# Optimization experiments

Hardware: AMD Instinct MI355X
Metric: run time of the kernel (lower is better)

## Reference

```python
import jax, jax.numpy as jnp
import numpy as np

HEAD = 8
C = 32  # dhead
SCALE = 0.17677669529663687  # 1/sqrt(32)


def setup_inputs() -> dict:
    key = jax.random.key(0)
    k1, k2, k3, k4 = jax.random.split(key, 4)
    N, S, R, M = 1, 256, 384, 256
    msa_repr = jax.random.normal(k1, (N, S, R, M), dtype=jnp.float32)
    # 0.02 init scale keeps softmax logits / sigmoid pre-activations in a sane range
    gate_proj = jax.random.normal(k2, (M, M), dtype=jnp.float32) * 0.02
    qkv_proj = jax.random.normal(k3, (M, 3 * M), dtype=jnp.float32) * 0.02
    out_proj = jax.random.normal(k4, (M, M), dtype=jnp.float32) * 0.02
    return {"msa_repr": msa_repr, "gate_proj": gate_proj, "qkv_proj": qkv_proj, "out_proj": out_proj}


def reference(msa_repr, gate_proj, qkv_proj, out_proj):
    # col_attn: permute [N,S,R,M] -> [N,R,S,M]; attention runs over the residue axis S
    x = jnp.transpose(msa_repr, (0, 2, 1, 3))  # [N,R,S,M]
    N, R, S, M = x.shape
    gate = jax.nn.sigmoid(x @ gate_proj).reshape(N, R, S, HEAD, C)
    q, k, v = jnp.split(x @ qkv_proj, 3, axis=-1)  # each [N,R,S,M]
    q = q.reshape(N, R, S, HEAD, C)
    k = k.reshape(N, R, S, HEAD, C)
    v = v.reshape(N, R, S, HEAD, C)
    sim = jnp.einsum('nrihc,nrjhc->nrhij', q, k) * jnp.float32(SCALE)  # [N,R,H,S,S]
    attn = jax.nn.softmax(sim, axis=-1)
    out = jnp.einsum('nrhij,nrjhc->nrihc', attn, v) * gate  # [N,R,S,H,C]
    out = out.reshape(N, R, S, HEAD * C) @ out_proj  # [N,R,S,M]
    return jnp.transpose(out, (0, 2, 1, 3))  # back to [N,S,R,M]
```

## Files before the change

### kernel.cpp

```cpp
#include <hip/hip_runtime.h>
#include <hip/hip_bf16.h>

#define R_DIM 384
#define S_DIM 256
#define M_DIM 256

typedef __attribute__((ext_vector_type(4))) float  f32x4;
typedef __attribute__((ext_vector_type(4))) float  fvec4;
typedef __attribute__((ext_vector_type(8))) short  short8;
typedef __attribute__((ext_vector_type(4))) short  short4v;

__device__ __forceinline__ short f2bf(float f) {
    __hip_bfloat16 h = __float2bfloat16(f);
    return __builtin_bit_cast(short, h);
}
__device__ __forceinline__ float bf2f(short s) {
    return __bfloat162float(__builtin_bit_cast(__hip_bfloat16, s));
}

#define QSCALE (0.17677669529663687f * 1.4426950408889634f)

__global__ __launch_bounds__(256) void k_prep(
    const float* __restrict__ gp, const float* __restrict__ qkvp,
    const float* __restrict__ op, short* __restrict__ Wt1,
    short* __restrict__ Wot)
{
    __shared__ float tile[64][65];
    const int tx = threadIdx.x & 63, ty = threadIdx.x >> 6;
    const int k0 = blockIdx.x * 64;
    const int j0 = blockIdx.y * 64;
    const float* src; int ld, cb;
    if (j0 < 256)       { src = gp;   ld = 256; cb = j0; }
    else if (j0 < 1024) { src = qkvp; ld = 768; cb = j0 - 256; }
    else                { src = op;   ld = 256; cb = j0 - 1024; }
    for (int q = 0; q < 16; ++q) {
        const int kk = q * 4 + ty;
        tile[kk][tx] = src[(k0 + kk) * ld + cb + tx];
    }
    __syncthreads();
    for (int q = 0; q < 16; ++q) {
        const int jj = q * 4 + ty;
        const int jglob = j0 + jj;
        const float scl = (jglob >= 256 && jglob < 512) ? QSCALE : 1.0f;
        const float val = tile[tx][jj] * scl;
        if (jglob < 1024) Wt1[jglob * 256 + k0 + tx] = f2bf(val);
        else              Wot[(jglob - 1024) * 256 + k0 + tx] = f2bf(val);
    }
}

__global__ __launch_bounds__(256) void k_qkvgate(
    const float* __restrict__ msa, const short* __restrict__ Wt1,
    short* __restrict__ gate, short* __restrict__ qb,
    short* __restrict__ kb, short* __restrict__ vb)
{
    __shared__ __align__(16) char Al[128 * 512];
    __shared__ __align__(16) char Bl[128 * 128];
    const int tid = threadIdx.x;
    const int l = tid & 63, w = tid >> 6;
    const int wr = w >> 1, wc = w & 1;
    const int rowBase = blockIdx.x * 128;

    {
        const int arow0 = tid >> 6;
        const int col4  = (tid & 63) * 4;
        const int slot  = (tid & 63) >> 1;
        const int sub   = (tid & 63) & 1;
        for (int ii = 0; ii < 32; ++ii) {
            const int a_r = ii * 4 + arow0;
            const int i = rowBase + a_r;
            const int rr = i >> 8, ss = i & 255;
            fvec4 vv = *(const fvec4*)(msa + ((ss * R_DIM + rr) << 8) + col4);
            short4v b4;
            b4.x = f2bf(vv.x); b4.y = f2bf(vv.y);
            b4.z = f2bf(vv.z); b4.w = f2bf(vv.w);
            *(short4v*)(Al + a_r * 512 + ((slot ^ (a_r & 7)) << 4) + sub * 8) = b4;
        }
    }
    __syncthreads();

    for (int ct = 0; ct < 8; ++ct) {
        const int colBase = ct * 128;
        f32x4 acc[4][4] = {};
        for (int kidx = 0; kidx < 4; ++kidx) {
            const int k0 = kidx * 64;
            {
                const int slotB = tid & 7;
                const int jb = tid >> 3;
                #pragma unroll
                for (int jj = 0; jj < 4; ++jj) {
                    const int j_r = jj * 32 + jb;
                    short8 wv = *(const short8*)(Wt1 + (colBase + j_r) * 256 + k0 + slotB * 8);
                    *(short8*)(Bl + j_r * 128 + ((slotB ^ (j_r & 7)) << 4)) = wv;
                }
            }
            __syncthreads();
            #pragma unroll
            for (int kh = 0; kh < 2; ++kh) {
                short8 af[4], bfr[4];
                const int aslot = kidx * 8 + kh * 4 + (l >> 4);
                const int bslot = kh * 4 + (l >> 4);
                #pragma unroll
                for (int it = 0; it < 4; ++it) {
                    const int row = wr * 64 + it * 16 + (l & 15);
                    af[it] = *(const short8*)(Al + row * 512 + ((aslot ^ (row & 7)) << 4));
                }
                #pragma unroll
                for (int jt = 0; jt < 4; ++jt) {
                    const int row = wc * 64 + jt * 16 + (l & 15);
                    bfr[jt] = *(const short8*)(Bl + row * 128 + ((bslot ^ (row & 7)) << 4));
                }
                #pragma unroll
                for (int it = 0; it < 4; ++it)
                    #pragma unroll
                    for (int jt = 0; jt < 4; ++jt)
                        acc[it][jt] = __builtin_amdgcn_mfma_f32_16x16x32_bf16(
                            af[it], bfr[jt], acc[it][jt], 0, 0, 0);
            }
            __syncthreads();
        }
        const int sel = ct >> 1;
        short* dst = (sel == 0) ? gate : (sel == 1) ? qb : (sel == 2) ? kb : vb;
        #pragma unroll
        for (int it = 0; it < 4; ++it) {
            const int base_i = rowBase + wr * 64 + it * 16 + ((l >> 4) << 2);
            #pragma unroll
            for (int reg = 0; reg < 4; ++reg) {
                const int i = base_i + reg;
                const int rr = i >> 8, ss = i & 255;
                #pragma unroll
                for (int jt = 0; jt < 4; ++jt) {
                    const int jg = colBase + wc * 64 + jt * 16 + (l & 15);
                    const int jj = jg & 255;
                    const int h = jj >> 5, c = jj & 31;
                    float vv = acc[it][jt][reg];
                    if (sel == 0) vv = 1.0f / (1.0f + __builtin_amdgcn_exp2f(-vv * 1.4426950408889634f));
                    dst[(((rr << 3) + h) * 256 + ss) * 32 + c] = f2bf(vv);
                }
            }
        }
    }
}

__global__ __launch_bounds__(256) void k_attn(
    short* qo, const short* __restrict__ kb, const short* __restrict__ vb,
    const short* __restrict__ gate)
{
    __shared__ __align__(16) short Kl[256 * 36];
    __shared__ __align__(16) short Vt[32 * 264];
    __shared__ __align__(16) short Pl[4 * 32 * 68];
    const int tid = threadIdx.x;
    const int l = tid & 63, w = tid >> 6;
    const int p = blockIdx.x;
    short* qg = qo + p * 8192;
    const short* kg = kb + p * 8192;
    const short* vg = vb + p * 8192;
    const short* gg = gate + p * 8192;

    short8 qf[4];
    {
        const int c0 = (l >> 4) * 8;
        #pragma unroll
        for (int it = 0; it < 4; ++it) {
            const int s = w * 64 + it * 16 + (l & 15);
            qf[it] = *(const short8*)(qg + s * 32 + c0);
        }
    }
    for (int itr = 0; itr < 4; ++itr) {
        const int idx = itr * 256 + tid;
        const int s = idx >> 2, slot = idx & 3;
        short8 kv = *(const short8*)(kg + s * 32 + slot * 8);
        *(short8*)(&Kl[s * 36 + slot * 8]) = kv;
    }
    for (int itr = 0; itr < 4; ++itr) {
        const int idx = itr * 256 + tid;
        const int s = idx >> 2, c0 = (idx & 3) * 8;
        short8 vv = *(const short8*)(vg + s * 32 + c0);
        #pragma unroll
        for (int e = 0; e < 8; ++e) Vt[(c0 + e) * 264 + s] = vv[e];
    }
    __syncthreads();

    f32x4 oacc[4][2] = {};
    f32x4 ssum[4] = {};
    short8 bones;
    #pragma unroll
    for (int e = 0; e < 8; ++e) bones[e] = (short)0x3F80;
    short* Pw = &Pl[w * (32 * 68)];

    for (int ch = 0; ch < 4; ++ch) {
        const int j0 = ch * 64;
        f32x4 sacc[4][4] = {};
        short8 kf[4];
        #pragma unroll
        for (int jt = 0; jt < 4; ++jt) {
            const int row = j0 + jt * 16 + (l & 15);
            kf[jt] = *(const short8*)(&Kl[row * 36 + (l >> 4) * 8]);
        }
        #pragma unroll
        for (int it = 0; it < 4; ++it)
            #pragma unroll
            for (int jt = 0; jt < 4; ++jt)
                sacc[it][jt] = __builtin_amdgcn_mfma_f32_16x16x32_bf16(
                    qf[it], kf[jt], sacc[it][jt], 0, 0, 0);

        short8 vfa[2][2];
        #pragma unroll
        for (int kk = 0; kk < 2; ++kk)
            #pragma unroll
            for (int cti = 0; cti < 2; ++cti)
                vfa[kk][cti] = *(const short8*)(
                    &Vt[(cti * 16 + (l & 15)) * 264 + j0 + kk * 32 + (l >> 4) * 8]);

        #pragma unroll
        for (int ih = 0; ih < 2; ++ih) {
            #pragma unroll
            for (int itl = 0; itl < 2; ++itl) {
                const int it = ih * 2 + itl;
                #pragma unroll
                for (int reg = 0; reg < 4; ++reg) {
                    const int rowl = itl * 16 + ((l >> 4) << 2) + reg;
                    #pragma unroll
                    for (int jt = 0; jt < 4; ++jt)
                        Pw[rowl * 68 + jt * 16 + (l & 15)] =
                            f2bf(__builtin_amdgcn_exp2f(sacc[it][jt][reg]));
                }
            }
            #pragma unroll
            for (int kk = 0; kk < 2; ++kk) {
                const int koff = kk * 32 + (l >> 4) * 8;
                short8 pf[2];
                #pragma unroll
                for (int itl = 0; itl < 2; ++itl)
                    pf[itl] = *(const short8*)(&Pw[(itl * 16 + (l & 15)) * 68 + koff]);
                #pragma unroll
                for (int itl = 0; itl < 2; ++itl) {
                    const int it = ih * 2 + itl;
                    #pragma unroll
                    for (int cti = 0; cti < 2; ++cti)
                        oacc[it][cti] = __builtin_amdgcn_mfma_f32_16x16x32_bf16(
                            pf[itl], vfa[kk][cti], oacc[it][cti], 0, 0, 0);
                    ssum[it] = __builtin_amdgcn_mfma_f32_16x16x32_bf16(
                        pf[itl], bones, ssum[it], 0, 0, 0);
                }
            }
        }
    }
    #pragma unroll
    for (int it = 0; it < 4; ++it) {
        #pragma unroll
        for (int reg = 0; reg < 4; ++reg) {
            const float inv = 1.0f / ssum[it][reg];
            const int s = w * 64 + it * 16 + ((l >> 4) << 2) + reg;
            #pragma unroll
            for (int cti = 0; cti < 2; ++cti) {
                const int c = cti * 16 + (l & 15);
                const float gv = bf2f(gg[s * 32 + c]);
                qg[s * 32 + c] = f2bf(oacc[it][cti][reg] * inv * gv);
            }
        }
    }
}

__global__ __launch_bounds__(256) void k_out(
    const short* __restrict__ ao, const short* __restrict__ Wot,
    float* __restrict__ out)
{
    __shared__ __align__(16) char Al[128 * 128];
    __shared__ __align__(16) char Bl[128 * 128];
    const int tid = threadIdx.x;
    const int l = tid & 63, w = tid >> 6;
    const int wr = w >> 1, wc = w & 1;
    const int rowBase = blockIdx.y * 128;
    const int colBase = blockIdx.x * 128;
    f32x4 acc[4][4] = {};
    for (int kidx = 0; kidx < 4; ++kidx) {
        const int k0 = kidx * 64;
        {
            const int slot = tid & 7;
            const int rb = tid >> 3;
            const int kin = k0 + slot * 8;
            const int h = kin >> 5, c0 = kin & 31;
            #pragma unroll
            for (int ii = 0; ii < 4; ++ii) {
                const int a_r = ii * 32 + rb;
                const int i = rowBase + a_r;
                const int rr = i >> 8, ss = i & 255;
                short8 av = *(const short8*)(ao + (((rr << 3) + h) * 256 + ss) * 32 + c0);
                *(short8*)(Al + a_r * 128 + ((slot ^ (a_r & 7)) << 4)) = av;
            }
            #pragma unroll
            for (int jj = 0; jj < 4; ++jj) {
                const int j_r = jj * 32 + rb;
                short8 wv = *(const short8*)(Wot + (colBase + j_r) * 256 + k0 + slot * 8);
                *(short8*)(Bl + j_r * 128 + ((slot ^ (j_r & 7)) << 4)) = wv;
            }
        }
        __syncthreads();
        #pragma unroll
        for (int kh = 0; kh < 2; ++kh) {
            short8 af[4], bfr[4];
            const int sl = kh * 4 + (l >> 4);
            #pragma unroll
            for (int it = 0; it < 4; ++it) {
                const int row = wr * 64 + it * 16 + (l & 15);
                af[it] = *(const short8*)(Al + row * 128 + ((sl ^ (row & 7)) << 4));
            }
            #pragma unroll
            for (int jt = 0; jt < 4; ++jt) {
                const int row = wc * 64 + jt * 16 + (l & 15);
                bfr[jt] = *(const short8*)(Bl + row * 128 + ((sl ^ (row & 7)) << 4));
            }
            #pragma unroll
            for (int it = 0; it < 4; ++it)
                #pragma unroll
                for (int jt = 0; jt < 4; ++jt)
                    acc[it][jt] = __builtin_amdgcn_mfma_f32_16x16x32_bf16(
                        af[it], bfr[jt], acc[it][jt], 0, 0, 0);
        }
        __syncthreads();
    }
    #pragma unroll
    for (int it = 0; it < 4; ++it) {
        const int base_i = rowBase + wr * 64 + it * 16 + ((l >> 4) << 2);
        #pragma unroll
        for (int reg = 0; reg < 4; ++reg) {
            const int i = base_i + reg;
            const int rr = i >> 8, ss = i & 255;
            #pragma unroll
            for (int jt = 0; jt < 4; ++jt) {
                const int m = colBase + wc * 64 + jt * 16 + (l & 15);
                out[((ss * R_DIM + rr) << 8) + m] = acc[it][jt][reg];
            }
        }
    }
}

extern "C" void kernel_launch(void* const* d_in, const int* in_sizes, int n_in,
                              void* d_out, int out_size, void* d_ws, size_t ws_size,
                              hipStream_t stream) {
    const float* msa  = (const float*)d_in[0];
    const float* gp   = (const float*)d_in[1];
    const float* qkvp = (const float*)d_in[2];
    const float* op   = (const float*)d_in[3];
    float* out = (float*)d_out;
    char* ws = (char*)d_ws;

    const size_t SZ = 50331648;
    short* Wt1  = (short*)ws;
    short* Wot  = (short*)(ws + 524288);
    short* gate = (short*)(ws + 655360);
    short* qb   = (short*)(ws + 655360 + 1 * SZ);
    short* kb   = (short*)(ws + 655360 + 2 * SZ);
    short* vb   = (short*)(ws + 655360 + 3 * SZ);

    k_prep<<<dim3(4, 20), 256, 0, stream>>>(gp, qkvp, op, Wt1, Wot);
    k_qkvgate<<<dim3(768), 256, 0, stream>>>(msa, Wt1, gate, qb, kb, vb);
    k_attn<<<dim3(3072), 256, 0, stream>>>(qb, kb, vb, gate);
    k_out<<<dim3(2, 768), 256, 0, stream>>>(qb, Wot, out);
}
```

Measured before the change: 245.1 us.

## Load QKV-gate weight fragments directly from global with register prefetch

The weight operand of the QKV/gate projection GEMM is no longer staged through a shared-memory tile. Each wave now loads its MFMA B fragments straight from global memory (L2-resident bf16 weights), prefetching the next k-step into registers. This removes two block-wide barriers per k-chunk and the LDS write/read traffic for B. In exchange every wave issues its own global loads for B, with some duplication across waves and more register pressure.

Result: slower. 276.5 us (+12.8%).

```diff
diff --git a/kernel.cpp b/kernel.cpp
--- a/kernel.cpp
+++ b/kernel.cpp
@@ -54,7 +54,6 @@
     short* __restrict__ kb, short* __restrict__ vb)
 {
     __shared__ __align__(16) char Al[128 * 512];
-    __shared__ __align__(16) char Bl[128 * 128];
     const int tid = threadIdx.x;
     const int l = tid & 63, w = tid >> 6;
     const int wr = w >> 1, wc = w & 1;
@@ -78,45 +77,38 @@
     }
     __syncthreads();
 
+    const short* Bbase = Wt1 + (wc * 64 + (l & 15)) * 256 + (l >> 4) * 8;
+
     for (int ct = 0; ct < 8; ++ct) {
         const int colBase = ct * 128;
         f32x4 acc[4][4] = {};
-        for (int kidx = 0; kidx < 4; ++kidx) {
-            const int k0 = kidx * 64;
-            {
-                const int slotB = tid & 7;
-                const int jb = tid >> 3;
-                #pragma unroll
-                for (int jj = 0; jj < 4; ++jj) {
-                    const int j_r = jj * 32 + jb;
-                    short8 wv = *(const short8*)(Wt1 + (colBase + j_r) * 256 + k0 + slotB * 8);
-                    *(short8*)(Bl + j_r * 128 + ((slotB ^ (j_r & 7)) << 4)) = wv;
-                }
-            }
-            __syncthreads();
-            #pragma unroll
-            for (int kh = 0; kh < 2; ++kh) {
-                short8 af[4], bfr[4];
-                const int aslot = kidx * 8 + kh * 4 + (l >> 4);
-                const int bslot = kh * 4 + (l >> 4);
-                #pragma unroll
-                for (int it = 0; it < 4; ++it) {
-                    const int row = wr * 64 + it * 16 + (l & 15);
-                    af[it] = *(const short8*)(Al + row * 512 + ((aslot ^ (row & 7)) << 4));
-                }
-                #pragma unroll
-                for (int jt = 0; jt < 4; ++jt) {
-                    const int row = wc * 64 + jt * 16 + (l & 15);
-                    bfr[jt] = *(const short8*)(Bl + row * 128 + ((bslot ^ (row & 7)) << 4));
-                }
-                #pragma unroll
-                for (int it = 0; it < 4; ++it)
-                    #pragma unroll
-                    for (int jt = 0; jt < 4; ++jt)
-                        acc[it][jt] = __builtin_amdgcn_mfma_f32_16x16x32_bf16(
-                            af[it], bfr[jt], acc[it][jt], 0, 0, 0);
-            }
-            __syncthreads();
+        short8 bcur[4], bnext[4];
+        #pragma unroll
+        for (int jt = 0; jt < 4; ++jt)
+            bnext[jt] = *(const short8*)(Bbase + (colBase + jt * 16) * 256);
+        #pragma unroll
+        for (int ks = 0; ks < 8; ++ks) {
+            #pragma unroll
+            for (int jt = 0; jt < 4; ++jt) bcur[jt] = bnext[jt];
+            if (ks < 7) {
+                const int ko = (ks + 1) * 32;
+                #pragma unroll
+                for (int jt = 0; jt < 4; ++jt)
+                    bnext[jt] = *(const short8*)(Bbase + (colBase + jt * 16) * 256 + ko);
+            }
+            short8 af[4];
+            const int aslot = ks * 4 + (l >> 4);
+            #pragma unroll
+            for (int it = 0; it < 4; ++it) {
+                const int row = wr * 64 + it * 16 + (l & 15);
+                af[it] = *(const short8*)(Al + row * 512 + ((aslot ^ (row & 7)) << 4));
+            }
+            #pragma unroll
+            for (int it = 0; it < 4; ++it)
+                #pragma unroll
+                for (int jt = 0; jt < 4; ++jt)
+                    acc[it][jt] = __builtin_amdgcn_mfma_f32_16x16x32_bf16(
+                        af[it], bcur[jt], acc[it][jt], 0, 0, 0);
         }
         const int sel = ct >> 1;
         short* dst = (sel == 0) ? gate : (sel == 1) ? qb : (sel == 2) ? kb : vb;
```

## Double-buffer weight tiles via direct global-to-LDS loads in QKV/gate GEMM

Applied to the files above, without the earlier changes.

Rewrites the B-operand staging of the QKV/gate projection kernel to use global_load_lds (direct global-to-LDS DMA) into a double-buffered 32-wide K slice. The loop is flattened over column tiles and K chunks, prefetching the next slice while computing the current one, which cuts per-chunk syncs. It also requests two blocks per CU via launch_bounds. This trades a smaller per-iteration K step and more iterations for overlap of weight loads with MFMA work. It adds the risk of register pressure under the occupancy hint, and a possible async-load hazard: the stores into LDS are never explicitly waited on before the barrier.

After: 252.1 us. +2.9%, slower.

```diff
diff --git a/kernel.cpp b/kernel.cpp
--- a/kernel.cpp
+++ b/kernel.cpp
@@ -16,6 +16,12 @@
 }
 __device__ __forceinline__ float bf2f(short s) {
     return __bfloat162float(__builtin_bit_cast(__hip_bfloat16, s));
+}
+
+__device__ __forceinline__ void gload_lds16(const void* gsrc, void* ldst) {
+    __builtin_amdgcn_global_load_lds(
+        (const __attribute__((address_space(1))) unsigned int*)gsrc,
+        (__attribute__((address_space(3))) unsigned int*)ldst, 16, 0, 0);
 }
 
 #define QSCALE (0.17677669529663687f * 1.4426950408889634f)
@@ -48,13 +54,13 @@
     }
 }
 
-__global__ __launch_bounds__(256) void k_qkvgate(
+__global__ __launch_bounds__(256, 2) void k_qkvgate(
     const float* __restrict__ msa, const short* __restrict__ Wt1,
     short* __restrict__ gate, short* __restrict__ qb,
     short* __restrict__ kb, short* __restrict__ vb)
 {
     __shared__ __align__(16) char Al[128 * 512];
-    __shared__ __align__(16) char Bl[128 * 128];
+    __shared__ __align__(16) short Bl[2][128 * 32];
     const int tid = threadIdx.x;
     const int l = tid & 63, w = tid >> 6;
     const int wr = w >> 1, wc = w & 1;
@@ -76,68 +82,78 @@
             *(short4v*)(Al + a_r * 512 + ((slot ^ (a_r & 7)) << 4) + sub * 8) = b4;
         }
     }
+
+    auto stageB = [&](int t) {
+        const int cb = (t >> 3) * 128, k0 = (t & 7) * 32;
+        short* buf = (short*)Bl[t & 1];
+        #pragma unroll
+        for (int r = 0; r < 2; ++r) {
+            const int L = r * 256 + w * 64 + l;
+            const int row = L >> 2, psl = L & 3;
+            const int gsl = psl ^ ((row >> 1) & 3);
+            gload_lds16(Wt1 + (cb + row) * 256 + k0 + gsl * 8,
+                        buf + (r * 256 + w * 64) * 8);
+        }
+    };
+
+    stageB(0);
     __syncthreads();
 
-    for (int ct = 0; ct < 8; ++ct) {
-        const int colBase = ct * 128;
-        f32x4 acc[4][4] = {};
-        for (int kidx = 0; kidx < 4; ++kidx) {
-            const int k0 = kidx * 64;
-            {
-                const int slotB = tid & 7;
-                const int jb = tid >> 3;
-                #pragma unroll
-                for (int jj = 0; jj < 4; ++jj) {
-                    const int j_r = jj * 32 + jb;
-                    short8 wv = *(const short8*)(Wt1 + (colBase + j_r) * 256 + k0 + slotB * 8);
-                    *(short8*)(Bl + j_r * 128 + ((slotB ^ (j_r & 7)) << 4)) = wv;
+    f32x4 acc[4][4] = {};
+    for (int t = 0; t < 64; ++t) {
+        const int ct = t >> 3, kc = t & 7;
+        if (t + 1 < 64) stageB(t + 1);
+
+        const short* Bb = (const short*)Bl[t & 1];
+        short8 af[4], bfr[4];
+        const int aslot = kc * 4 + (l >> 4);
+        #pragma unroll
+        for (int it = 0; it < 4; ++it) {
+            const int row = wr * 64 + it * 16 + (l & 15);
+            af[it] = *(const short8*)(Al + row * 512 + ((aslot ^ (row & 7)) << 4));
+        }
+        #pragma unroll
+        for (int jt = 0; jt < 4; ++jt) {
+            const int row = wc * 64 + jt * 16 + (l & 15);
+            const int psl = (l >> 4) ^ ((row >> 1) & 3);
+            bfr[jt] = *(const short8*)(Bb + row * 32 + psl * 8);
+        }
+        #pragma unroll
+        for (int it = 0; it < 4; ++it)
+            #pragma unroll
+            for (int jt = 0; jt < 4; ++jt)
+                acc[it][jt] = __builtin_amdgcn_mfma_f32_16x16x32_bf16(
+                    af[it], bfr[jt], acc[it][jt], 0, 0, 0);
+
+        if (kc == 7) {
+            const int colBase = ct * 128;
+            const int sel = ct >> 1;
+            short* dst = (sel == 0) ? gate : (sel == 1) ? qb : (sel == 2) ? kb : vb;
+            #pragma unroll
+            for (int it = 0; it < 4; ++it) {
+                const int base_i = rowBase + wr * 64 + it * 16 + ((l >> 4) << 2);
+                #pragma unroll
+                for (int reg = 0; reg < 4; ++reg) {
+                    const int i = base_i + reg;
+                    const int rr = i >> 8, ss = i & 255;
+                    #pragma unroll
+                    for (int jt = 0; jt < 4; ++jt) {
+                        const int jg = colBase + wc * 64 + jt * 16 + (l & 15);
+                        const int jj = jg & 255;
+                        const int h = jj >> 5, c = jj & 31;
+                        float vv = acc[it][jt][reg];
+                        if (sel == 0) vv = 1.0f / (1.0f + __builtin_amdgcn_exp2f(-vv * 1.4426950408889634f));
+                        dst[(((rr << 3) + h) * 256 + ss) * 32 + c] = f2bf(vv);
+                    }
                 }
             }
-            __syncthreads();
-            #pragma unroll
-            for (int kh = 0; kh < 2; ++kh) {
-                short8 af[4], bfr[4];
-                const int aslot = kidx * 8 + kh * 4 + (l >> 4);
-                const int bslot = kh * 4 + (l >> 4);
-                #pragma unroll
-                for (int it = 0; it < 4; ++it) {
-                    const int row = wr * 64 + it * 16 + (l & 15);
-                    af[it] = *(const short8*)(Al + row * 512 + ((aslot ^ (row & 7)) << 4));
-                }
-                #pragma unroll
-                for (int jt = 0; jt < 4; ++jt) {
-                    const int row = wc * 64 + jt * 16 + (l & 15);
-                    bfr[jt] = *(const short8*)(Bl + row * 128 + ((bslot ^ (row & 7)) << 4));
-                }
-                #pragma unroll
-                for (int it = 0; it < 4; ++it)
-                    #pragma unroll
-                    for (int jt = 0; jt < 4; ++jt)
-                        acc[it][jt] = __builtin_amdgcn_mfma_f32_16x16x32_bf16(
-                            af[it], bfr[jt], acc[it][jt], 0, 0, 0);
-            }
-            __syncthreads();
-        }
-        const int sel = ct >> 1;
-        short* dst = (sel == 0) ? gate : (sel == 1) ? qb : (sel == 2) ? kb : vb;
-        #pragma unroll
-        for (int it = 0; it < 4; ++it) {
-            const int base_i = rowBase + wr * 64 + it * 16 + ((l >> 4) << 2);
-            #pragma unroll
-            for (int reg = 0; reg < 4; ++reg) {
-                const int i = base_i + reg;
-                const int rr = i >> 8, ss = i & 255;
-                #pragma unroll
-                for (int jt = 0; jt < 4; ++jt) {
-                    const int jg = colBase + wc * 64 + jt * 16 + (l & 15);
-                    const int jj = jg & 255;
-                    const int h = jj >> 5, c = jj & 31;
-                    float vv = acc[it][jt][reg];
-                    if (sel == 0) vv = 1.0f / (1.0f + __builtin_amdgcn_exp2f(-vv * 1.4426950408889634f));
-                    dst[(((rr << 3) + h) * 256 + ss) * 32 + c] = f2bf(vv);
-                }
-            }
-        }
+            #pragma unroll
+            for (int it = 0; it < 4; ++it)
+                #pragma unroll
+                for (int jt = 0; jt < 4; ++jt)
+                    acc[it][jt] = (f32x4){0.f, 0.f, 0.f, 0.f};
+        }
+        __syncthreads();
     }
 }
 
```
